# Performance work log

Measured on AMD Instinct MI355X. Metric: run time of the kernel, lower is better.

The kernel has to match this reference:

```python
import jax, jax.numpy as jnp
import numpy as np

B, L, H, E, V, T = 64, 512, 512, 512, 64, 200  # L must equal H (attention broadcast in source)
SOS_TOKEN = 0


def setup_inputs() -> dict:
    key = jax.random.key(0)
    ks = jax.random.split(key, 16)
    s = 0.05
    return {
        "seq_embeddings": jax.random.normal(ks[0], (B, L, H), jnp.float32),
        "key_w": jax.random.normal(ks[1], (H, H), jnp.float32) * s,
        "key_b": jax.random.normal(ks[2], (H,), jnp.float32) * s,
        "value_w": jax.random.normal(ks[3], (H, H), jnp.float32) * s,
        "value_b": jax.random.normal(ks[4], (H,), jnp.float32) * s,
        "char_emb": jax.random.normal(ks[5], (V, E), jnp.float32) * s,
        "w_ih": jax.random.normal(ks[6], (4 * H, E + H), jnp.float32) * s,
        "w_hh": jax.random.normal(ks[7], (4 * H, H), jnp.float32) * s,
        "b_ih": jax.random.normal(ks[8], (4 * H,), jnp.float32) * s,
        "b_hh": jax.random.normal(ks[9], (4 * H,), jnp.float32) * s,
        "cdn_w": jax.random.normal(ks[10], (V, 2 * H), jnp.float32) * s,
        "cdn_b": jax.random.normal(ks[11], (V,), jnp.float32) * s,
        "seq_embedding_lengths": jax.random.randint(ks[12], (B,), 1, L + 1),
        "batch_y": jax.random.randint(ks[13], (B, T), 0, V),
    }


def reference(seq_embeddings, key_w, key_b, value_w, value_b, char_emb,
              w_ih, w_hh, b_ih, b_hh, cdn_w, cdn_b,
              seq_embedding_lengths, batch_y):
    b, l, h = seq_embeddings.shape
    t = batch_y.shape[1]
    v = cdn_w.shape[0]
    dt = seq_embeddings.dtype

    # Attention: since logits = sum_l (keys*q) and context = sum_l (values*w),
    # both factor through the masked sum over L -> precompute once (loop-invariant).
    mask = (jnp.arange(l)[None, :] < seq_embedding_lengths[:, None]).astype(dt)  # (B, L)
    msum = jnp.einsum('blh,bl->bh', seq_embeddings, mask)                        # (B, H)
    keysum = msum @ key_w.T + l * key_b                                          # sum of keys over L
    valsum = msum @ value_w.T + l * value_b                                      # sum of values over L
    scale = jnp.sqrt(jnp.asarray(h, dt))

    def attend(q):  # q: (B, H); softmax over the key_dim axis, as in source
        w = jax.nn.softmax(keysum * q / scale, axis=1)
        return valsum * w

    ctx0 = attend(jnp.zeros((b, h), dt))
    h0 = jnp.zeros((b, h), dt)
    c0 = jnp.zeros((b, h), dt)

    # prev token at step i: SOS at i=1, batch_y[:, i-1] afterwards (tf_rate=1.0)
    prev_ys = jnp.concatenate(
        [jnp.full((1, b), SOS_TOKEN, dtype=batch_y.dtype), batch_y[:, 1:t - 1].T], axis=0)  # (T-1, B)

    def step(carry, y_prev):
        hh, cc, ctx = carry
        x = jnp.concatenate([char_emb[y_prev], ctx], axis=1)           # (B, E+H)
        gates = x @ w_ih.T + b_ih + hh @ w_hh.T + b_hh                 # (B, 4H)
        i_g, f_g, g_g, o_g = jnp.split(gates, 4, axis=1)
        cc = jax.nn.sigmoid(f_g) * cc + jax.nn.sigmoid(i_g) * jnp.tanh(g_g)
        hh = jax.nn.sigmoid(o_g) * jnp.tanh(cc)
        ctx = attend(hh)
        logit = jnp.concatenate([hh, ctx], axis=1) @ cdn_w.T + cdn_b   # (B, V)
        return (hh, cc, ctx), logit

    _, logits_seq = jax.lax.scan(step, (h0, c0, ctx0), prev_ys)        # (T-1, B, V)
    logits = jnp.concatenate(
        [jnp.zeros((1, b, v), dt), logits_seq], axis=0).transpose(1, 0, 2)  # (B, T, V)

    # multinomial sampling of output symbols (random in source; seeded here)
    samp = jax.random.categorical(jax.random.key(1), logits[:, 1:, :], axis=-1)
    symbols = jnp.concatenate(
        [jnp.zeros((b, 1), samp.dtype), samp], axis=1)                 # (B, T)
    return logits, symbols
```

## Files before the change

### kernel.cpp

```cpp
#include <hip/hip_runtime.h>
#include <math.h>

#define NB 64
#define NH 512
#define NV 64
#define NT 200
#define NSTEP 199
#define GBLK 256
#define GTHR 512

#define RLX   __ATOMIC_RELAXED
#define AGENT __HIP_MEMORY_SCOPE_AGENT
#define WGRP  __HIP_MEMORY_SCOPE_WORKGROUP

typedef float f4v __attribute__((ext_vector_type(4)));

__device__ inline float gumbel_tf(unsigned f){
  const unsigned ksc[3] = {0u, 1u, 0x1BD11BDBu};
  unsigned x0 = 0u + ksc[0];
  unsigned x1 = f  + ksc[1];
  const int R0[4] = {13,15,26,6};
  const int R1[4] = {17,29,16,24};
  #pragma unroll
  for (int i = 0; i < 5; ++i){
    #pragma unroll
    for (int r = 0; r < 4; ++r){
      int rot = (i & 1) ? R1[r] : R0[r];
      x0 += x1;
      x1 = (x1 << rot) | (x1 >> (32 - rot));
      x1 ^= x0;
    }
    x0 += ksc[(i+1)%3];
    x1 += ksc[(i+2)%3] + (unsigned)(i+1);
  }
  unsigned bits = x0 ^ x1;
  float u = __uint_as_float((bits >> 9) | 0x3F800000u) - 1.0f;
  u = fmaxf(u, 1.17549435e-38f);
  return -logf(-logf(u));
}

__device__ inline float sigf(float x){ return 1.0f/(1.0f + expf(-x)); }

__device__ inline void poll256(unsigned* flags, unsigned tgt){
  const int l = threadIdx.x & 63;
  #pragma unroll
  for (int j = 0; j < 4; ++j){
    while (__hip_atomic_load(&flags[(l*4 + j)*16], RLX, AGENT) < tgt){
      __builtin_amdgcn_s_sleep(1);
    }
  }
}

__device__ inline float blk_red_max(float v, float* scr){
  #pragma unroll
  for (int m = 1; m < 64; m <<= 1) v = fmaxf(v, __shfl_xor(v, m, 64));
  if ((threadIdx.x & 63) == 0) scr[threadIdx.x >> 6] = v;
  __syncthreads();
  float r = scr[0];
  #pragma unroll
  for (int i = 1; i < 8; ++i) r = fmaxf(r, scr[i]);
  __syncthreads();
  return r;
}
__device__ inline float blk_red_sum(float v, float* scr){
  #pragma unroll
  for (int m = 1; m < 64; m <<= 1) v += __shfl_xor(v, m, 64);
  if ((threadIdx.x & 63) == 0) scr[threadIdx.x >> 6] = v;
  __syncthreads();
  float r = 0.f;
  #pragma unroll
  for (int i = 0; i < 8; ++i) r += scr[i];
  __syncthreads();
  return r;
}

__global__ void k_msum_part(const float* __restrict__ emb, const int* __restrict__ lens,
                            float* __restrict__ part){
  int blk = blockIdx.x, b = blk >> 3, lc = blk & 7;
  int len = lens[b];
  int l0 = lc*64, l1 = len < l0+64 ? len : l0+64;
  for (int h = threadIdx.x; h < 512; h += 256){
    float a = 0.f;
    for (int l = l0; l < l1; ++l) a += emb[(b*512 + l)*512 + h];
    part[blk*512 + h] = a;
  }
}
__global__ void k_msum(const float* __restrict__ part, float* __restrict__ msumT){
  int b = blockIdx.x;
  for (int h = threadIdx.x; h < 512; h += 256){
    float a = 0.f;
    #pragma unroll
    for (int lc = 0; lc < 8; ++lc) a += part[(b*8+lc)*512 + h];
    msumT[h*64 + b] = a;
  }
}
__global__ void k_kv(const float* __restrict__ msumT,
                     const float* __restrict__ kw, const float* __restrict__ kb,
                     const float* __restrict__ vw, const float* __restrict__ vb,
                     float* __restrict__ keysum, float* __restrict__ valsum){
  int which = blockIdx.x >> 7;
  int i = ((blockIdx.x & 127) << 2) + (threadIdx.x >> 6);
  int b = threadIdx.x & 63;
  const float* W = which ? vw : kw;
  float a = 0.f;
  for (int h = 0; h < 512; ++h) a = fmaf(msumT[h*64+b], W[i*512+h], a);
  float bias = which ? vb[i] : kb[i];
  float* out = which ? valsum : keysum;
  out[b*512 + i] = a + 512.0f*bias;
}
__global__ void k_ceT(const float* __restrict__ ce, float* __restrict__ ceT){
  int idx = blockIdx.x*256 + threadIdx.x;
  if (idx < 32768){ int v = idx >> 9, e = idx & 511; ceT[e*64 + v] = ce[v*512 + e]; }
}
__global__ void k_tok(const float* __restrict__ ceT, const float* __restrict__ w_ih,
                      const float* __restrict__ b_ih, const float* __restrict__ b_hh,
                      float* __restrict__ tok){
  int idx = blockIdx.x*256 + threadIdx.x;
  int v = idx & 63, row = idx >> 6;
  float a = 0.f;
  for (int e = 0; e < 512; ++e) a = fmaf(ceT[e*64+v], w_ih[row*1024 + e], a);
  tok[v*2048 + row] = a + b_ih[row] + b_hh[row];
}
__global__ void k_init(const float* __restrict__ valsum, const float* __restrict__ cdn_w,
                       float* __restrict__ cdnT, float* __restrict__ xT,
                       float* __restrict__ out, unsigned* __restrict__ bar){
  int idx = blockIdx.x*256 + threadIdx.x;
  if (idx < 65536){
    int v = idx >> 10, k = idx & 1023;
    cdnT[k*64 + v] = cdn_w[idx];
  } else if (idx < 98304){
    int r = idx - 65536; int j = r >> 6, b = r & 63;
    xT[j*64 + b] = valsum[b*512 + j] * (1.0f/512.0f);
  } else if (idx < 131072){
    xT[idx - 65536] = 0.f;
  } else if (idx < 135168){
    int r = idx - 131072; int b = r >> 6, v = r & 63;
    out[b*12800 + v] = 0.f;
  } else if (idx < 135232){
    int b = idx - 135168;
    out[819200 + b*200] = 0.f;
  } else if (idx < 139392){
    bar[idx - 135232] = 0u;
  }
}

__global__ __launch_bounds__(GTHR, 2) void k_loop(
    const float* __restrict__ w_ih, const float* __restrict__ w_hh,
    const int* __restrict__ batch_y, const float* __restrict__ tok,
    const float* __restrict__ keysum, const float* __restrict__ valsum,
    const float* __restrict__ cdnT, const float* __restrict__ cdn_b,
    float* __restrict__ xT, float* __restrict__ out,
    unsigned* __restrict__ flags){
  __shared__ float W_lds[1024][8];
  __shared__ float red[8][8][64];
  __shared__ float gates_lds[8][64];
  __shared__ float cc_lds[2][64];
  __shared__ float pb_h[512], pb_c[512];
  __shared__ float pb_lp[8][64];
  __shared__ float scr[8];
  __shared__ int done_h, done_c, done_pb;

  const int tid = threadIdx.x;
  const int blk = blockIdx.x;
  const bool HASB = (blk < 64);

  if (tid == 0){ done_h = 0; done_c = 0; done_pb = 0; }
  for (int idx = tid; idx < 8192; idx += GTHR){
    int k = idx >> 3, r = idx & 7;
    int g = r >> 1, c = r & 1;
    int row = g*512 + blk*2 + c;
    W_lds[k][r] = (k < 512) ? w_ih[row*1024 + 512 + k] : w_hh[row*512 + (k - 512)];
  }
  if (tid < 128) cc_lds[tid >> 6][tid & 63] = 0.0f;
  __syncthreads();

  const int w = tid >> 6, l = tid & 63, kg = l >> 4, bg = l & 15;
  const float SCALE = 22.627416997969522f;

#define ISS1(R, JJ) do{ const float* _p = xin + (((kbase + (JJ)*4) << 6) | (bg << 2)); \
  asm volatile("global_load_dwordx4 %0, %1, off sc0 sc1" : "=v"(R) : "v"(_p)); }while(0)
#define ISS8(P, J0) do{ ISS1(P##0,(J0)+0);ISS1(P##1,(J0)+1);ISS1(P##2,(J0)+2);ISS1(P##3,(J0)+3); \
  ISS1(P##4,(J0)+4);ISS1(P##5,(J0)+5);ISS1(P##6,(J0)+6);ISS1(P##7,(J0)+7); }while(0)
#define CMP1(R, JJ) do{ int _k = kbase + (JJ)*4; \
  f4v _wA = *(const f4v*)&W_lds[_k][0]; f4v _wB = *(const f4v*)&W_lds[_k][4]; \
  float _wv[8] = {_wA.x,_wA.y,_wA.z,_wA.w,_wB.x,_wB.y,_wB.z,_wB.w}; \
  float _xv[4] = {R.x,R.y,R.z,R.w}; \
  _Pragma("unroll") for (int _r = 0; _r < 8; ++_r){ \
    _Pragma("unroll") for (int _q = 0; _q < 4; ++_q) \
      acc[_r][_q] = fmaf(_wv[_r], _xv[_q], acc[_r][_q]); } }while(0)
#define CMP8(P, J0) do{ CMP1(P##0,(J0)+0);CMP1(P##1,(J0)+1);CMP1(P##2,(J0)+2);CMP1(P##3,(J0)+3); \
  CMP1(P##4,(J0)+4);CMP1(P##5,(J0)+5);CMP1(P##6,(J0)+6);CMP1(P##7,(J0)+7); }while(0)
#define WAITV(N) do{ asm volatile("s_waitcnt vmcnt(" #N ")" ::: "memory"); \
  __builtin_amdgcn_sched_barrier(0); }while(0)

  for (int s = 0; s < NSTEP; ++s){
    const float* xin  = xT + (size_t)(s & 1)*65536;
    float*       xout = xT + (size_t)((s + 1) & 1)*65536;
    const unsigned t1 = (unsigned)(2*s + 1), t2 = (unsigned)(2*s + 2);
    const unsigned tgt_h = (s == 0) ? 0u : (unsigned)(2*s - 1);
    const unsigned tgt_c = (s == 0) ? 0u : (unsigned)(2*s);

    if (w >= 4){
      if (w == 4){
        poll256(flags, tgt_h);
        __hip_atomic_store(&done_h, s + 1, RLX, WGRP);
      } else {
        while (__hip_atomic_load(&done_h, RLX, WGRP) < s + 1){
          __builtin_amdgcn_s_sleep(1);
        }
      }
    } else {
      if (w == 0){
        poll256(flags, tgt_c);
        __hip_atomic_store(&done_c, s + 1, RLX, WGRP);
      } else {
        while (__hip_atomic_load(&done_c, RLX, WGRP) < s + 1){
          __builtin_amdgcn_s_sleep(1);
        }
      }
    }

    const int rr = tid >> 6, rb = tid & 63;
    int yprev = (s == 0) ? 0 : batch_y[rb*200 + s];
    float tokval = tok[yprev*2048 + (rr >> 1)*512 + blk*2 + (rr & 1)];

    float acc[8][4];
    #pragma unroll
    for (int r = 0; r < 8; ++r)
      #pragma unroll
      for (int q = 0; q < 4; ++q) acc[r][q] = 0.f;

    const int kbase = w*128 + kg;
    {
      f4v A0,A1,A2,A3,A4,A5,A6,A7,B0,B1,B2,B3,B4,B5,B6,B7;
      ISS8(A, 0);
      ISS8(B, 8);
      WAITV(8); CMP8(A, 0);
      ISS8(A, 16);
      WAITV(8); CMP8(B, 8);
      ISS8(B, 24);
      WAITV(8); CMP8(A, 16);
      WAITV(0); CMP8(B, 24);
    }

    #pragma unroll
    for (int r = 0; r < 8; ++r)
      #pragma unroll
      for (int q = 0; q < 4; ++q){
        float v = acc[r][q];
        v += __shfl_xor(v, 16, 64);
        v += __shfl_xor(v, 32, 64);
        acc[r][q] = v;
      }
    if (l < 16){
      #pragma unroll
      for (int r = 0; r < 8; ++r)
        *(float4*)&red[w][r][bg*4] = make_float4(acc[r][0], acc[r][1], acc[r][2], acc[r][3]);
    }
    __syncthreads();
    {
      float g = 0.f;
      #pragma unroll
      for (int ww = 0; ww < 8; ++ww) g += red[ww][rr][rb];
      gates_lds[rr][rb] = g + tokval;
    }
    __syncthreads();
    if (tid < 128){
      int c = tid >> 6, b = tid & 63;
      float ig = gates_lds[0 + c][b];
      float fg = gates_lds[2 + c][b];
      float gg = gates_lds[4 + c][b];
      float og = gates_lds[6 + c][b];
      float cprev = cc_lds[c][b];
      float cnew = sigf(fg)*cprev + sigf(ig)*tanhf(gg);
      float hnew = sigf(og)*tanhf(cnew);
      cc_lds[c][b] = cnew;
      float oldh = __hip_atomic_exchange(&xout[(512 + blk*2 + c)*64 + b], hnew, RLX, AGENT);
      asm volatile("" :: "v"(oldh));
    }

    asm volatile("s_waitcnt vmcnt(0)" ::: "memory");
    __syncthreads();
    if (tid == 0){
      unsigned o = __hip_atomic_exchange(&flags[blk*16], HASB ? t1 : t2, RLX, AGENT);
      asm volatile("" :: "v"(o));
    }

    if (HASB){
      if (w == 4){
        poll256(flags, t1);
        __hip_atomic_store(&done_pb, s + 1, RLX, WGRP);
      } else {
        while (__hip_atomic_load(&done_pb, RLX, WGRP) < s + 1){
          __builtin_amdgcn_s_sleep(1);
        }
      }

      int b = blk;
      int jj = tid;
      float h = __hip_atomic_load(&xout[(512 + jj)*64 + b], RLX, AGENT);
      pb_h[jj] = h;
      float sc = (keysum[b*512 + jj] * h) / SCALE;
      float m = blk_red_max(sc, scr);
      float e = expf(sc - m);
      float S = blk_red_sum(e, scr);
      float cx = valsum[b*512 + jj] * (e / S);
      pb_c[jj] = cx;
      float oldc = __hip_atomic_exchange(&xout[jj*64 + b], cx, RLX, AGENT);
      asm volatile("" :: "v"(oldc));
      __syncthreads();
      int kq = tid >> 6, v = tid & 63;
      float part = 0.f;
      for (int k = kq*128; k < kq*128 + 128; ++k){
        float xh = (k < 512) ? pb_h[k] : pb_c[k - 512];
        part = fmaf(cdnT[k*64 + v], xh, part);
      }
      pb_lp[kq][v] = part;
      __syncthreads();
      if (tid < 64){
        int v2 = tid;
        float logit = cdn_b[v2];
        #pragma unroll
        for (int q = 0; q < 8; ++q) logit += pb_lp[q][v2];
        out[b*12800 + (s+1)*64 + v2] = logit;
        float z = gumbel_tf((unsigned)((b*199 + s)*64 + v2)) + logit;
        int idx = v2;
        #pragma unroll
        for (int mm = 1; mm < 64; mm <<= 1){
          float oz = __shfl_xor(z, mm, 64);
          int   oi = __shfl_xor(idx, mm, 64);
          if (oz > z || (oz == z && oi < idx)){ z = oz; idx = oi; }
        }
        if (v2 == 0) out[819200 + b*200 + (s+1)] = (float)idx;
      }

      asm volatile("s_waitcnt vmcnt(0)" ::: "memory");
      __syncthreads();
      if (tid == 0){
        unsigned o = __hip_atomic_exchange(&flags[blk*16], t2, RLX, AGENT);
        asm volatile("" :: "v"(o));
      }
    }
  }
#undef ISS1
#undef ISS8
#undef CMP1
#undef CMP8
#undef WAITV
}

extern "C" void kernel_launch(void* const* d_in, const int* in_sizes, int n_in,
                              void* d_out, int out_size, void* d_ws, size_t ws_size,
                              hipStream_t stream){
  const float* seq     = (const float*)d_in[0];
  const float* key_w   = (const float*)d_in[1];
  const float* key_b   = (const float*)d_in[2];
  const float* value_w = (const float*)d_in[3];
  const float* value_b = (const float*)d_in[4];
  const float* char_e  = (const float*)d_in[5];
  const float* w_ih    = (const float*)d_in[6];
  const float* w_hh    = (const float*)d_in[7];
  const float* b_ih    = (const float*)d_in[8];
  const float* b_hh    = (const float*)d_in[9];
  const float* cdn_w   = (const float*)d_in[10];
  const float* cdn_b   = (const float*)d_in[11];
  const int*   lens    = (const int*)d_in[12];
  const int*   batch_y = (const int*)d_in[13];
  float* out = (float*)d_out;
  float* ws  = (float*)d_ws;

  float* msum_part = ws;
  float* msumT     = ws + 262144;
  float* keysum    = ws + 294912;
  float* valsum    = ws + 327680;
  float* tok       = ws + 360448;
  float* cdnT      = ws + 491520;
  float* ceT       = ws + 557056;
  float* xT        = ws + 589824;
  unsigned* bar    = (unsigned*)(ws + 720896);

  k_msum_part<<<512, 256, 0, stream>>>(seq, lens, msum_part);
  k_msum     <<<64,  256, 0, stream>>>(msum_part, msumT);
  k_kv       <<<256, 256, 0, stream>>>(msumT, key_w, key_b, value_w, value_b, keysum, valsum);
  k_ceT      <<<128, 256, 0, stream>>>(char_e, ceT);
  k_tok      <<<512, 256, 0, stream>>>(ceT, w_ih, b_ih, b_hh, tok);
  k_init     <<<545, 256, 0, stream>>>(valsum, cdn_w, cdnT, xT, out, bar);

  k_loop<<<GBLK, GTHR, 0, stream>>>(w_ih, w_hh, batch_y, tok, keysum, valsum,
                                    cdnT, cdn_b, xT, out, bar);
  (void)in_sizes; (void)n_in; (void)out_size; (void)ws_size;
}
```

Measured before the change: 5.922 ms.

## Mirror recurrent state into per-XCC copies to cut cross-die coherent loads

Adds per-XCC mirror buffers of the hidden/context state. Each step, one block per XCC wins a claim, waits for all blocks to finish, and copies the new state into its XCC's mirror. Other blocks then poll one mirror flag and read the mirror with non-system-coherent loads instead of polling 256 flags and doing sc0 sc1 loads. This aims to replace expensive coherent cross-die traffic with L2-local reads. The cost is an extra serialized copy stage and wait on the critical path of each step. The mode is chosen from the workspace size.

```diff
diff --git a/kernel.cpp b/kernel.cpp
--- a/kernel.cpp
+++ b/kernel.cpp
@@ -49,6 +49,14 @@
       __builtin_amdgcn_s_sleep(1);
     }
   }
+}
+__device__ inline void gwait_all(unsigned* flags, unsigned tgt){
+  if (threadIdx.x < 256){
+    while (__hip_atomic_load(&flags[threadIdx.x*16], RLX, AGENT) < tgt){
+      __builtin_amdgcn_s_sleep(1);
+    }
+  }
+  __syncthreads();
 }
 
 __device__ inline float blk_red_max(float v, float* scr){
@@ -139,50 +147,21 @@
   } else if (idx < 135232){
     int b = idx - 135168;
     out[819200 + b*200] = 0.f;
-  } else if (idx < 139392){
+  } else if (idx < 139584){
     bar[idx - 135232] = 0u;
   }
 }
 
-__global__ __launch_bounds__(GTHR, 2) void k_loop(
-    const float* __restrict__ w_ih, const float* __restrict__ w_hh,
-    const int* __restrict__ batch_y, const float* __restrict__ tok,
-    const float* __restrict__ keysum, const float* __restrict__ valsum,
-    const float* __restrict__ cdnT, const float* __restrict__ cdn_b,
-    float* __restrict__ xT, float* __restrict__ out,
-    unsigned* __restrict__ flags){
-  __shared__ float W_lds[1024][8];
-  __shared__ float red[8][8][64];
-  __shared__ float gates_lds[8][64];
-  __shared__ float cc_lds[2][64];
-  __shared__ float pb_h[512], pb_c[512];
-  __shared__ float pb_lp[8][64];
-  __shared__ float scr[8];
-  __shared__ int done_h, done_c, done_pb;
-
-  const int tid = threadIdx.x;
-  const int blk = blockIdx.x;
-  const bool HASB = (blk < 64);
-
-  if (tid == 0){ done_h = 0; done_c = 0; done_pb = 0; }
-  for (int idx = tid; idx < 8192; idx += GTHR){
-    int k = idx >> 3, r = idx & 7;
-    int g = r >> 1, c = r & 1;
-    int row = g*512 + blk*2 + c;
-    W_lds[k][r] = (k < 512) ? w_ih[row*1024 + 512 + k] : w_hh[row*512 + (k - 512)];
-  }
-  if (tid < 128) cc_lds[tid >> 6][tid & 63] = 0.0f;
-  __syncthreads();
-
-  const int w = tid >> 6, l = tid & 63, kg = l >> 4, bg = l & 15;
-  const float SCALE = 22.627416997969522f;
-
-#define ISS1(R, JJ) do{ const float* _p = xin + (((kbase + (JJ)*4) << 6) | (bg << 2)); \
-  asm volatile("global_load_dwordx4 %0, %1, off sc0 sc1" : "=v"(R) : "v"(_p)); }while(0)
+template<bool COH>
+__device__ __forceinline__ void pipeA(const float* base, const float (*W)[8],
+                                      int kbase, int bg, float acc[8][4]){
+#define ISS1(R, JJ) do{ const float* _p = base + (((kbase + (JJ)*4) << 6) | (bg << 2)); \
+  if (COH) asm volatile("global_load_dwordx4 %0, %1, off sc0 sc1" : "=v"(R) : "v"(_p)); \
+  else     asm volatile("global_load_dwordx4 %0, %1, off sc0"     : "=v"(R) : "v"(_p)); }while(0)
 #define ISS8(P, J0) do{ ISS1(P##0,(J0)+0);ISS1(P##1,(J0)+1);ISS1(P##2,(J0)+2);ISS1(P##3,(J0)+3); \
   ISS1(P##4,(J0)+4);ISS1(P##5,(J0)+5);ISS1(P##6,(J0)+6);ISS1(P##7,(J0)+7); }while(0)
 #define CMP1(R, JJ) do{ int _k = kbase + (JJ)*4; \
-  f4v _wA = *(const f4v*)&W_lds[_k][0]; f4v _wB = *(const f4v*)&W_lds[_k][4]; \
+  f4v _wA = *(const f4v*)&W[_k][0]; f4v _wB = *(const f4v*)&W[_k][4]; \
   float _wv[8] = {_wA.x,_wA.y,_wA.z,_wA.w,_wB.x,_wB.y,_wB.z,_wB.w}; \
   float _xv[4] = {R.x,R.y,R.z,R.w}; \
   _Pragma("unroll") for (int _r = 0; _r < 8; ++_r){ \
@@ -192,31 +171,97 @@
   CMP1(P##4,(J0)+4);CMP1(P##5,(J0)+5);CMP1(P##6,(J0)+6);CMP1(P##7,(J0)+7); }while(0)
 #define WAITV(N) do{ asm volatile("s_waitcnt vmcnt(" #N ")" ::: "memory"); \
   __builtin_amdgcn_sched_barrier(0); }while(0)
+  f4v A0,A1,A2,A3,A4,A5,A6,A7,B0,B1,B2,B3,B4,B5,B6,B7;
+  ISS8(A, 0);
+  ISS8(B, 8);
+  WAITV(8); CMP8(A, 0);
+  ISS8(A, 16);
+  WAITV(8); CMP8(B, 8);
+  ISS8(B, 24);
+  WAITV(8); CMP8(A, 16);
+  WAITV(0); CMP8(B, 24);
+#undef ISS1
+#undef ISS8
+#undef CMP1
+#undef CMP8
+#undef WAITV
+}
+
+template<int MODE>
+__global__ __launch_bounds__(GTHR, 2) void k_loop(
+    const float* __restrict__ w_ih, const float* __restrict__ w_hh,
+    const int* __restrict__ batch_y, const float* __restrict__ tok,
+    const float* __restrict__ keysum, const float* __restrict__ valsum,
+    const float* __restrict__ cdnT, const float* __restrict__ cdn_b,
+    float* __restrict__ xT, float* __restrict__ mir,
+    float* __restrict__ out, unsigned* __restrict__ bar){
+  __shared__ float W_lds[1024][8];
+  __shared__ float red[8][8][64];
+  __shared__ float gates_lds[8][64];
+  __shared__ float cc_lds[2][64];
+  __shared__ float pb_h[512], pb_c[512];
+  __shared__ float pb_lp[8][64];
+  __shared__ float scr[8];
+  __shared__ int done_h, done_c, done_pb;
+  __shared__ int swin;
+
+  unsigned* flags = bar;
+  unsigned* claim = bar + 4096;
+  unsigned* mflag = bar + 4224;
+
+  const int tid = threadIdx.x;
+  const int blk = blockIdx.x;
+  const bool HASB = (blk < 64);
+
+  unsigned xcc = 0;
+  asm("s_getreg_b32 %0, hwreg(HW_REG_XCC_ID)" : "=s"(xcc));
+  xcc &= 7u;
+  float* mymir = mir + (size_t)xcc * (MODE == 2 ? 65536 : 32768);
+  const float* mbase = (MODE == 2) ? mymir : (mymir - 32768);
+
+  if (tid == 0){ done_h = 0; done_c = 0; done_pb = 0; swin = 0; }
+  for (int idx = tid; idx < 8192; idx += GTHR){
+    int k = idx >> 3, r = idx & 7;
+    int g = r >> 1, c = r & 1;
+    int row = g*512 + blk*2 + c;
+    W_lds[k][r] = (k < 512) ? w_ih[row*1024 + 512 + k] : w_hh[row*512 + (k - 512)];
+  }
+  if (tid < 128) cc_lds[tid >> 6][tid & 63] = 0.0f;
+  __syncthreads();
+
+  const int w = tid >> 6, l = tid & 63, kg = l >> 4, bg = l & 15;
+  const float SCALE = 22.627416997969522f;
 
   for (int s = 0; s < NSTEP; ++s){
     const float* xin  = xT + (size_t)(s & 1)*65536;
     float*       xout = xT + (size_t)((s + 1) & 1)*65536;
     const unsigned t1 = (unsigned)(2*s + 1), t2 = (unsigned)(2*s + 2);
+    const unsigned tgt_c = (s == 0) ? 0u : (unsigned)(2*s);
     const unsigned tgt_h = (s == 0) ? 0u : (unsigned)(2*s - 1);
-    const unsigned tgt_c = (s == 0) ? 0u : (unsigned)(2*s);
 
     if (w >= 4){
       if (w == 4){
-        poll256(flags, tgt_h);
+        if (MODE >= 1 && s > 0){
+          while (__hip_atomic_load(&mflag[xcc*16], RLX, AGENT) < (unsigned)s)
+            __builtin_amdgcn_s_sleep(1);
+        } else {
+          poll256(flags, tgt_h);
+        }
         __hip_atomic_store(&done_h, s + 1, RLX, WGRP);
       } else {
-        while (__hip_atomic_load(&done_h, RLX, WGRP) < s + 1){
-          __builtin_amdgcn_s_sleep(1);
-        }
+        while (__hip_atomic_load(&done_h, RLX, WGRP) < s + 1) __builtin_amdgcn_s_sleep(1);
       }
     } else {
       if (w == 0){
-        poll256(flags, tgt_c);
+        if (MODE == 2 && s > 0){
+          while (__hip_atomic_load(&mflag[xcc*16], RLX, AGENT) < (unsigned)s)
+            __builtin_amdgcn_s_sleep(1);
+        } else {
+          poll256(flags, tgt_c);
+        }
         __hip_atomic_store(&done_c, s + 1, RLX, WGRP);
       } else {
-        while (__hip_atomic_load(&done_c, RLX, WGRP) < s + 1){
-          __builtin_amdgcn_s_sleep(1);
-        }
+        while (__hip_atomic_load(&done_c, RLX, WGRP) < s + 1) __builtin_amdgcn_s_sleep(1);
       }
     }
 
@@ -231,17 +276,9 @@
       for (int q = 0; q < 4; ++q) acc[r][q] = 0.f;
 
     const int kbase = w*128 + kg;
-    {
-      f4v A0,A1,A2,A3,A4,A5,A6,A7,B0,B1,B2,B3,B4,B5,B6,B7;
-      ISS8(A, 0);
-      ISS8(B, 8);
-      WAITV(8); CMP8(A, 0);
-      ISS8(A, 16);
-      WAITV(8); CMP8(B, 8);
-      ISS8(B, 24);
-      WAITV(8); CMP8(A, 16);
-      WAITV(0); CMP8(B, 24);
-    }
+    const bool use_mir = (s > 0) && (MODE == 2 || (MODE == 1 && w >= 4));
+    if (use_mir) pipeA<false>(mbase, W_lds, kbase, bg, acc);
+    else         pipeA<true >(xin,   W_lds, kbase, bg, acc);
 
     #pragma unroll
     for (int r = 0; r < 8; ++r)
@@ -291,9 +328,7 @@
         poll256(flags, t1);
         __hip_atomic_store(&done_pb, s + 1, RLX, WGRP);
       } else {
-        while (__hip_atomic_load(&done_pb, RLX, WGRP) < s + 1){
-          __builtin_amdgcn_s_sleep(1);
-        }
+        while (__hip_atomic_load(&done_pb, RLX, WGRP) < s + 1) __builtin_amdgcn_s_sleep(1);
       }
 
       int b = blk;
@@ -341,12 +376,42 @@
         asm volatile("" :: "v"(o));
       }
     }
-  }
-#undef ISS1
-#undef ISS8
-#undef CMP1
-#undef CMP8
-#undef WAITV
+
+    if (MODE >= 1 && s < NSTEP - 1){
+      if (tid == 0){
+        unsigned exp = (unsigned)s;
+        bool win = __hip_atomic_compare_exchange_strong(&claim[xcc*16], &exp,
+                     (unsigned)(s + 1), RLX, RLX, AGENT);
+        swin = win ? 1 : 0;
+      }
+      __syncthreads();
+      if (swin){
+        gwait_all(flags, (MODE == 2) ? t2 : t1);
+        const float* src = xout + ((MODE == 2) ? 0 : 32768);
+        float*       dst = mymir;
+        const int per = (MODE == 2) ? 32 : 16;
+        f4v buf0,buf1,buf2,buf3,buf4,buf5,buf6,buf7;
+        for (int j0 = 0; j0 < per; j0 += 8){
+#define CLD(R, J) do{ const float* _sp = src + (size_t)(((j0+(J))*GTHR + tid))*4; \
+  asm volatile("global_load_dwordx4 %0, %1, off sc0 sc1" : "=v"(R) : "v"(_sp)); }while(0)
+#define CST(R, J) do{ *(f4v*)(dst + (size_t)(((j0+(J))*GTHR + tid))*4) = R; }while(0)
+          CLD(buf0,0); CLD(buf1,1); CLD(buf2,2); CLD(buf3,3);
+          CLD(buf4,4); CLD(buf5,5); CLD(buf6,6); CLD(buf7,7);
+          asm volatile("s_waitcnt vmcnt(0)" ::: "memory");
+          CST(buf0,0); CST(buf1,1); CST(buf2,2); CST(buf3,3);
+          CST(buf4,4); CST(buf5,5); CST(buf6,6); CST(buf7,7);
+#undef CLD
+#undef CST
+        }
+        asm volatile("s_waitcnt vmcnt(0)" ::: "memory");
+        __syncthreads();
+        if (tid == 0){
+          unsigned o = __hip_atomic_exchange(&mflag[xcc*16], (unsigned)(s + 1), RLX, AGENT);
+          asm volatile("" :: "v"(o));
+        }
+      }
+    }
+  }
 }
 
 extern "C" void kernel_launch(void* const* d_in, const int* in_sizes, int n_in,
@@ -369,24 +434,34 @@
   float* out = (float*)d_out;
   float* ws  = (float*)d_ws;
 
+  const size_t wsw = ws_size / sizeof(float);
+  const bool M2 = (wsw >= 922112);
+  const size_t B = M2 ? 524288 : 262144;
+
+  float* mir       = ws;
   float* msum_part = ws;
-  float* msumT     = ws + 262144;
-  float* keysum    = ws + 294912;
-  float* valsum    = ws + 327680;
-  float* tok       = ws + 360448;
-  float* cdnT      = ws + 491520;
-  float* ceT       = ws + 557056;
-  float* xT        = ws + 589824;
-  unsigned* bar    = (unsigned*)(ws + 720896);
+  float* keysum    = ws + B;
+  float* valsum    = ws + B + 32768;
+  float* tok       = ws + B + 65536;
+  float* cdnT      = ws + B + 196608;
+  float* xT        = ws + B + 262144;
+  unsigned* bar    = (unsigned*)(ws + B + 393216);
+  float* msumT     = M2 ? (ws + 262144) : (ws + B + 397568);
+  float* ceT       = M2 ? (ws + 294912) : (ws);
 
   k_msum_part<<<512, 256, 0, stream>>>(seq, lens, msum_part);
   k_msum     <<<64,  256, 0, stream>>>(msum_part, msumT);
   k_kv       <<<256, 256, 0, stream>>>(msumT, key_w, key_b, value_w, value_b, keysum, valsum);
   k_ceT      <<<128, 256, 0, stream>>>(char_e, ceT);
   k_tok      <<<512, 256, 0, stream>>>(ceT, w_ih, b_ih, b_hh, tok);
-  k_init     <<<545, 256, 0, stream>>>(valsum, cdn_w, cdnT, xT, out, bar);
-
-  k_loop<<<GBLK, GTHR, 0, stream>>>(w_ih, w_hh, batch_y, tok, keysum, valsum,
-                                    cdnT, cdn_b, xT, out, bar);
+  k_init     <<<546, 256, 0, stream>>>(valsum, cdn_w, cdnT, xT, out, bar);
+
+  if (M2){
+    k_loop<2><<<GBLK, GTHR, 0, stream>>>(w_ih, w_hh, batch_y, tok, keysum, valsum,
+                                         cdnT, cdn_b, xT, mir, out, bar);
+  } else {
+    k_loop<1><<<GBLK, GTHR, 0, stream>>>(w_ih, w_hh, batch_y, tok, keysum, valsum,
+                                         cdnT, cdn_b, xT, mir, out, bar);
+  }
   (void)in_sizes; (void)n_in; (void)out_size; (void)ws_size;
 }
```

New measurement: 13.04 ms. +120.2%, slower.

## Move output projection and sampling to separate blocks, lagged one step

Applied to the files above, without the earlier changes.

The per-batch attention blocks now only compute the context and signal completion. The output projection, logit write and Gumbel sampling move to blocks 64-127, which handle step s-1 during step s using a triple-buffered transposed h and a double-buffered ctx in workspace. This takes the projection off the recurrent critical path. The context wait now polls only the 64 attention-block flags instead of all 256. In exchange it adds extra global atomic writes per step, an epilogue for the last step, and workspace buffers that alias msum_part, which is safe only because that data is dead by then.

```diff
diff --git a/kernel.cpp b/kernel.cpp
--- a/kernel.cpp
+++ b/kernel.cpp
@@ -48,6 +48,12 @@
     while (__hip_atomic_load(&flags[(l*4 + j)*16], RLX, AGENT) < tgt){
       __builtin_amdgcn_s_sleep(1);
     }
+  }
+}
+__device__ inline void poll64(unsigned* flags, unsigned tgt){
+  const int l = threadIdx.x & 63;
+  while (__hip_atomic_load(&flags[l*16], RLX, AGENT) < tgt){
+    __builtin_amdgcn_s_sleep(1);
   }
 }
 
@@ -139,7 +145,7 @@
   } else if (idx < 135232){
     int b = idx - 135168;
     out[819200 + b*200] = 0.f;
-  } else if (idx < 139392){
+  } else if (idx < 139328){
     bar[idx - 135232] = 0u;
   }
 }
@@ -149,8 +155,8 @@
     const int* __restrict__ batch_y, const float* __restrict__ tok,
     const float* __restrict__ keysum, const float* __restrict__ valsum,
     const float* __restrict__ cdnT, const float* __restrict__ cdn_b,
-    float* __restrict__ xT, float* __restrict__ out,
-    unsigned* __restrict__ flags){
+    float* __restrict__ xT, float* __restrict__ hT3, float* __restrict__ ctxT,
+    float* __restrict__ out, unsigned* __restrict__ flags){
   __shared__ float W_lds[1024][8];
   __shared__ float red[8][8][64];
   __shared__ float gates_lds[8][64];
@@ -163,6 +169,7 @@
   const int tid = threadIdx.x;
   const int blk = blockIdx.x;
   const bool HASB = (blk < 64);
+  const bool HASL = (blk >= 64 && blk < 128);
 
   if (tid == 0){ done_h = 0; done_c = 0; done_pb = 0; }
   for (int idx = tid; idx < 8192; idx += GTHR){
@@ -205,18 +212,14 @@
         poll256(flags, tgt_h);
         __hip_atomic_store(&done_h, s + 1, RLX, WGRP);
       } else {
-        while (__hip_atomic_load(&done_h, RLX, WGRP) < s + 1){
-          __builtin_amdgcn_s_sleep(1);
-        }
+        while (__hip_atomic_load(&done_h, RLX, WGRP) < s + 1) __builtin_amdgcn_s_sleep(1);
       }
     } else {
       if (w == 0){
-        poll256(flags, tgt_c);
+        poll64(flags, tgt_c);
         __hip_atomic_store(&done_c, s + 1, RLX, WGRP);
       } else {
-        while (__hip_atomic_load(&done_c, RLX, WGRP) < s + 1){
-          __builtin_amdgcn_s_sleep(1);
-        }
+        while (__hip_atomic_load(&done_c, RLX, WGRP) < s + 1) __builtin_amdgcn_s_sleep(1);
       }
     }
 
@@ -277,6 +280,9 @@
       cc_lds[c][b] = cnew;
       float oldh = __hip_atomic_exchange(&xout[(512 + blk*2 + c)*64 + b], hnew, RLX, AGENT);
       asm volatile("" :: "v"(oldh));
+      float oldt = __hip_atomic_exchange(
+          &hT3[(size_t)((s + 1) % 3)*32768 + b*512 + (blk*2 + c)], hnew, RLX, AGENT);
+      asm volatile("" :: "v"(oldt));
     }
 
     asm volatile("s_waitcnt vmcnt(0)" ::: "memory");
@@ -291,23 +297,44 @@
         poll256(flags, t1);
         __hip_atomic_store(&done_pb, s + 1, RLX, WGRP);
       } else {
-        while (__hip_atomic_load(&done_pb, RLX, WGRP) < s + 1){
-          __builtin_amdgcn_s_sleep(1);
-        }
+        while (__hip_atomic_load(&done_pb, RLX, WGRP) < s + 1) __builtin_amdgcn_s_sleep(1);
       }
 
       int b = blk;
       int jj = tid;
-      float h = __hip_atomic_load(&xout[(512 + jj)*64 + b], RLX, AGENT);
+      float h;
+      { const float* hp = hT3 + (size_t)((s + 1) % 3)*32768 + b*512 + jj;
+        asm volatile("global_load_dword %0, %1, off sc0 sc1" : "=v"(h) : "v"(hp));
+        asm volatile("s_waitcnt vmcnt(0)" ::: "memory"); }
       pb_h[jj] = h;
       float sc = (keysum[b*512 + jj] * h) / SCALE;
       float m = blk_red_max(sc, scr);
       float e = expf(sc - m);
       float S = blk_red_sum(e, scr);
       float cx = valsum[b*512 + jj] * (e / S);
-      pb_c[jj] = cx;
       float oldc = __hip_atomic_exchange(&xout[jj*64 + b], cx, RLX, AGENT);
       asm volatile("" :: "v"(oldc));
+      float oldt = __hip_atomic_exchange(&ctxT[(size_t)(s & 1)*32768 + b*512 + jj], cx, RLX, AGENT);
+      asm volatile("" :: "v"(oldt));
+      asm volatile("s_waitcnt vmcnt(0)" ::: "memory");
+      __syncthreads();
+      if (tid == 0){
+        unsigned o = __hip_atomic_exchange(&flags[blk*16], t2, RLX, AGENT);
+        asm volatile("" :: "v"(o));
+      }
+    }
+
+    if (HASL && s >= 1){
+      int b = blk - 64;
+      int sp = s - 1;
+      float h, c;
+      { const float* hp = hT3 + (size_t)(s % 3)*32768 + b*512 + tid;
+        const float* cp = ctxT + (size_t)(sp & 1)*32768 + b*512 + tid;
+        asm volatile("global_load_dword %0, %1, off sc0 sc1" : "=v"(h) : "v"(hp));
+        asm volatile("global_load_dword %0, %1, off sc0 sc1" : "=v"(c) : "v"(cp));
+        asm volatile("s_waitcnt vmcnt(0)" ::: "memory"); }
+      pb_h[tid] = h;
+      pb_c[tid] = c;
       __syncthreads();
       int kq = tid >> 6, v = tid & 63;
       float part = 0.f;
@@ -322,8 +349,8 @@
         float logit = cdn_b[v2];
         #pragma unroll
         for (int q = 0; q < 8; ++q) logit += pb_lp[q][v2];
-        out[b*12800 + (s+1)*64 + v2] = logit;
-        float z = gumbel_tf((unsigned)((b*199 + s)*64 + v2)) + logit;
+        out[b*12800 + (sp+1)*64 + v2] = logit;
+        float z = gumbel_tf((unsigned)((b*199 + sp)*64 + v2)) + logit;
         int idx = v2;
         #pragma unroll
         for (int mm = 1; mm < 64; mm <<= 1){
@@ -331,15 +358,51 @@
           int   oi = __shfl_xor(idx, mm, 64);
           if (oz > z || (oz == z && oi < idx)){ z = oz; idx = oi; }
         }
-        if (v2 == 0) out[819200 + b*200 + (s+1)] = (float)idx;
-      }
-
-      asm volatile("s_waitcnt vmcnt(0)" ::: "memory");
-      __syncthreads();
-      if (tid == 0){
-        unsigned o = __hip_atomic_exchange(&flags[blk*16], t2, RLX, AGENT);
-        asm volatile("" :: "v"(o));
-      }
+        if (v2 == 0) out[819200 + b*200 + (sp+1)] = (float)idx;
+      }
+    }
+  }
+
+  if (HASL){
+    int b = blk - 64;
+    const int sp = NSTEP - 1;
+    if (tid == 0){
+      while (__hip_atomic_load(&flags[b*16], RLX, AGENT) < (unsigned)(2*sp + 2))
+        __builtin_amdgcn_s_sleep(1);
+    }
+    __syncthreads();
+    float h, c;
+    { const float* hp = hT3 + (size_t)((sp + 1) % 3)*32768 + b*512 + tid;
+      const float* cp = ctxT + (size_t)(sp & 1)*32768 + b*512 + tid;
+      asm volatile("global_load_dword %0, %1, off sc0 sc1" : "=v"(h) : "v"(hp));
+      asm volatile("global_load_dword %0, %1, off sc0 sc1" : "=v"(c) : "v"(cp));
+      asm volatile("s_waitcnt vmcnt(0)" ::: "memory"); }
+    pb_h[tid] = h;
+    pb_c[tid] = c;
+    __syncthreads();
+    int kq = tid >> 6, v = tid & 63;
+    float part = 0.f;
+    for (int k = kq*128; k < kq*128 + 128; ++k){
+      float xh = (k < 512) ? pb_h[k] : pb_c[k - 512];
+      part = fmaf(cdnT[k*64 + v], xh, part);
+    }
+    pb_lp[kq][v] = part;
+    __syncthreads();
+    if (tid < 64){
+      int v2 = tid;
+      float logit = cdn_b[v2];
+      #pragma unroll
+      for (int q = 0; q < 8; ++q) logit += pb_lp[q][v2];
+      out[b*12800 + (sp+1)*64 + v2] = logit;
+      float z = gumbel_tf((unsigned)((b*199 + sp)*64 + v2)) + logit;
+      int idx = v2;
+      #pragma unroll
+      for (int mm = 1; mm < 64; mm <<= 1){
+        float oz = __shfl_xor(z, mm, 64);
+        int   oi = __shfl_xor(idx, mm, 64);
+        if (oz > z || (oz == z && oi < idx)){ z = oz; idx = oi; }
+      }
+      if (v2 == 0) out[819200 + b*200 + (sp+1)] = (float)idx;
     }
   }
 #undef ISS1
@@ -369,6 +432,8 @@
   float* out = (float*)d_out;
   float* ws  = (float*)d_ws;
 
+  float* hT3       = ws;
+  float* ctxT      = ws + 98304;
   float* msum_part = ws;
   float* msumT     = ws + 262144;
   float* keysum    = ws + 294912;
@@ -387,6 +452,6 @@
   k_init     <<<545, 256, 0, stream>>>(valsum, cdn_w, cdnT, xT, out, bar);
 
   k_loop<<<GBLK, GTHR, 0, stream>>>(w_ih, w_hh, batch_y, tok, keysum, valsum,
-                                    cdnT, cdn_b, xT, out, bar);
+                                    cdnT, cdn_b, xT, hT3, ctxT, out, bar);
   (void)in_sizes; (void)n_in; (void)out_size; (void)ws_size;
 }
```

Measured after the change: 4.811 ms (median of 2 runs). 18.8% less time.
